# Performance work log

Hardware: AMD Instinct MI355X
Metric: run time of the kernel (lower is better)

## Reference

```python
import jax, jax.numpy as jnp
import numpy as np

CHUNK_SIZE = 256


def setup_inputs() -> dict:
    key = jax.random.key(0)
    kq, kk, kv = jax.random.split(key, 3)
    b, h, L, d, dv = 2, 16, 4096, 16, 64
    return {
        "q": jax.random.normal(kq, (b, h, L, d), dtype=jnp.float32),
        "k": jax.random.normal(kk, (b, h, L, d), dtype=jnp.float32),
        "v": jax.random.normal(kv, (b, h, L, dv), dtype=jnp.float32),
    }


def reference(q, k, v):
    b, h, L, d = q.shape
    dv = v.shape[-1]
    cs = CHUNK_SIZE
    n = L // cs

    q = q * d ** (-0.5)

    # ---- normalizer z over full sequence ----
    k_cumsum = jnp.cumsum(k, axis=-2)                               # [b,h,L,d]
    kk_cumsum = jnp.cumsum(k[..., :, None] * k[..., None, :], axis=-3)  # [b,h,L,d,d]
    z = (q * k_cumsum).sum(-1)
    z = z + 0.5 * jnp.einsum('bhld,bhle,bhlde->bhl', q, q, kk_cumsum)
    z = z + (jnp.arange(L, dtype=z.dtype) + 1.0)[None, None, :]

    # ---- zeroth-order term ----
    o_const = jnp.cumsum(v, axis=-2)                                # [b,h,L,dv]

    # ---- chunked view ----
    qc = q.reshape(b, h, n, cs, d)
    kc = k.reshape(b, h, n, cs, d)
    vc = v.reshape(b, h, n, cs, dv)

    # intra-chunk quadratic attention: S + 0.5*S^2, causal-masked
    s = jnp.einsum('bhnqd,bhnkd->bhnqk', qc, kc)                    # [b,h,n,cs,cs]
    s = s + 0.5 * s ** 2
    causal_mask = jnp.tril(jnp.ones((cs, cs), dtype=bool))
    s = jnp.where(causal_mask, s, jnp.zeros((), dtype=s.dtype))
    o = jnp.einsum('bhnqk,bhnkf->bhnqf', s, vc)                     # [b,h,n,cs,dv]

    # inter-chunk quadratic state: cumulative K x K x V from previous chunks
    kv_quad = jnp.einsum('bhncd,bhnce,bhncf->bhndef', kc, kc, vc)   # [b,h,n,d,d,dv]
    kv_quad = jnp.cumsum(kv_quad, axis=2)
    kv_quad = jnp.concatenate(
        [jnp.zeros_like(kv_quad[:, :, :1]), kv_quad[:, :, :-1]], axis=2)
    o = o + 0.5 * jnp.einsum('bhndef,bhncd,bhnce->bhncf', kv_quad, qc, qc)

    # inter-chunk linear state: cumulative K x V from previous chunks
    kv_lin = jnp.einsum('bhncd,bhnce->bhnde', kc, vc)               # [b,h,n,d,dv]
    kv_lin = jnp.cumsum(kv_lin, axis=2)
    kv_lin = jnp.concatenate(
        [jnp.zeros_like(kv_lin[:, :, :1]), kv_lin[:, :, :-1]], axis=2)
    o = o + jnp.einsum('bhnde,bhncd->bhnce', kv_lin, qc)

    o = o.reshape(b, h, L, dv) + o_const
    return o / (z[..., None] + 1e-6)
```

## Files before the change

kernel.cpp:

```cpp
#include <hip/hip_runtime.h>
#include <hip/hip_cooperative_groups.h>
#include <cstddef>

#define BH    32
#define LSEQ  4096
#define D     16
#define DV    64
#define CS    256
#define NC    16
#define NF    160
#define NZ    65
#define KSTEPS 5
#define PER   (NZ * NF)

typedef short short8 __attribute__((ext_vector_type(8)));
typedef float f32x4 __attribute__((ext_vector_type(4)));

#define OFF_KBF 0u
#define OFF_VT  (4u*1024u*1024u)
#define OFF_ST  (OFF_VT + (unsigned)(BH*NZ*LSEQ*2))

__device__ __forceinline__ unsigned f2bf(float x) {
  unsigned u = __float_as_uint(x);
  return (u + 0x7FFFu + ((u >> 16) & 1u)) >> 16;
}
__device__ __forceinline__ float bf2f(unsigned short u) {
  return __uint_as_float(((unsigned)u) << 16);
}
__device__ __forceinline__ short8 zero8() {
  short8 z = {0,0,0,0,0,0,0,0};
  return z;
}

__device__ __forceinline__ unsigned feat_tbl(int f) {
  if (f == 0)  return 16u | (16u << 8);
  if (f <= 16) return (unsigned)(f - 1) | (16u << 8);
  if (f < 137) {
    int p = f - 17, off = 0;
    for (int d = 0; d < 15; ++d) {
      int cnt = 15 - d;
      if (p < off + cnt) return (unsigned)d | ((unsigned)(d + 1 + p - off) << 8);
      off += cnt;
    }
  }
  if (f < 153) {
    int d = f - 137;
    return (unsigned)d | ((unsigned)d << 8) | (1u << 16);
  }
  return 17u | (17u << 8);
}

struct Smem {
  float kxqx[CS][18];
  __align__(16) unsigned short vt[NZ][264];
  union {
    __align__(16) unsigned short stt[NZ][168];
    struct {
      __align__(16) unsigned short ptile[8][1280];
      float zline[CS];
    } u;
  } b;
  unsigned tbl[NF];
};

__global__ __launch_bounds__(512, 4) void unified(const float* __restrict__ q,
                                                  const float* __restrict__ k,
                                                  const float* __restrict__ v,
                                                  unsigned* __restrict__ kbf_u32,
                                                  unsigned short* __restrict__ st,
                                                  float* __restrict__ out) {
  __shared__ Smem sm;
  int blk = blockIdx.x, bh = blk >> 4, c = blk & 15;
  int t = threadIdx.x, w = t >> 6, lane = t & 63, quad = lane >> 4, n16 = lane & 15;
  const size_t base = (size_t)bh * LSEQ + (size_t)c * CS;

  {
    const float2* kc2 = (const float2*)(k + base * D);
    unsigned* kbd = kbf_u32 + base * D / 2;
    for (int i = t; i < 2048; i += 512) {
      float2 v2 = kc2[i];
      kbd[i] = f2bf(v2.x) | (f2bf(v2.y) << 16);
      int j = i >> 3, dd = (i & 7) * 2;
      sm.kxqx[j][dd] = v2.x; sm.kxqx[j][dd + 1] = v2.y;
    }
    for (int i = t; i < CS; i += 512) { sm.kxqx[i][16] = 1.f; sm.kxqx[i][17] = 0.f; }
    const float* vb = v + base * DV;
    for (int i = t; i < CS * DV; i += 512) {
      int j = i >> 6, f = i & 63;
      sm.vt[f][j] = (unsigned short)f2bf(vb[i]);
    }
    for (int i = t; i < CS; i += 512) sm.vt[64][i] = (unsigned short)0x3F80;
    if (t < NF) sm.tbl[t] = feat_tbl(t);
  }
  __syncthreads();

  if (c < 15 && w < 5) {
    f32x4 acc[2][5];
#pragma unroll
    for (int mm = 0; mm < 2; ++mm)
#pragma unroll
      for (int nt = 0; nt < 5; ++nt) acc[mm][nt] = (f32x4){0.f, 0.f, 0.f, 0.f};
    for (int jt = 0; jt < 8; ++jt) {
      short8 afr[2];
#pragma unroll
      for (int mm = 0; mm < 2; ++mm) {
        int feat = (w * 2 + mm) * 16 + n16;
        unsigned tv = sm.tbl[feat];
        int d = tv & 255, e = (tv >> 8) & 255;
        short8 a;
#pragma unroll
        for (int i = 0; i < 8; ++i) {
          int jj = jt * 32 + quad * 8 + i;
          a[i] = (short)f2bf(sm.kxqx[jj][d] * sm.kxqx[jj][e]);
        }
        afr[mm] = a;
      }
#pragma unroll
      for (int nt = 0; nt < 5; ++nt) {
        int ncol = nt * 16 + n16;
        short8 b = zero8();
        if (ncol < NZ) b = *(const short8*)(&sm.vt[ncol][jt * 32 + quad * 8]);
        acc[0][nt] = __builtin_amdgcn_mfma_f32_16x16x32_bf16(afr[0], b, acc[0][nt], 0, 0, 0);
        acc[1][nt] = __builtin_amdgcn_mfma_f32_16x16x32_bf16(afr[1], b, acc[1][nt], 0, 0, 0);
      }
    }
    unsigned short* stc = st + (size_t)(bh * NC + c) * PER;
#pragma unroll
    for (int mm = 0; mm < 2; ++mm)
#pragma unroll
      for (int nt = 0; nt < 5; ++nt) {
        int col = nt * 16 + n16;
        if (col < NZ) {
          unsigned lo = f2bf(acc[mm][nt][0]) | (f2bf(acc[mm][nt][1]) << 16);
          unsigned hi = f2bf(acc[mm][nt][2]) | (f2bf(acc[mm][nt][3]) << 16);
          int feat0 = (w * 2 + mm) * 16 + quad * 4;
          *(uint2*)(stc + (size_t)col * NF + feat0) = make_uint2(lo, hi);
        }
      }
  }
  __syncthreads();

  {
    const float* qc = q + base * D;
    for (int i = t; i < CS * D; i += 512) {
      int row = i >> 4, dd = i & 15;
      sm.kxqx[row][dd] = qc[i] * 0.25f;
    }
  }

  cooperative_groups::this_grid().sync();

  if (c > 0) {
    const unsigned short* stg = st + (size_t)bh * NC * PER;
    float s0[8], s1[8], s2[8];
#pragma unroll
    for (int e = 0; e < 8; ++e) { s0[e] = 0.f; s1[e] = 0.f; s2[e] = 0.f; }
    const int i0 = t * 8, i1 = i0 + 4096, i2 = i0 + 8192;
    const bool h2 = (i2 < PER);
    for (int cc = 0; cc < c; ++cc) {
      const unsigned short* pcc = stg + (size_t)cc * PER;
      short8 a0 = *(const short8*)(pcc + i0);
      short8 a1 = *(const short8*)(pcc + i1);
      short8 a2 = h2 ? *(const short8*)(pcc + i2) : zero8();
#pragma unroll
      for (int e = 0; e < 8; ++e) {
        s0[e] += bf2f((unsigned short)a0[e]);
        s1[e] += bf2f((unsigned short)a1[e]);
        s2[e] += bf2f((unsigned short)a2[e]);
      }
    }
    {
      int col = i0 / NF, ft = i0 - col * NF;
      short8 p;
#pragma unroll
      for (int e = 0; e < 8; ++e) p[e] = (short)f2bf(s0[e]);
      *(short8*)(&sm.b.stt[col][ft]) = p;
      col = i1 / NF; ft = i1 - col * NF;
#pragma unroll
      for (int e = 0; e < 8; ++e) p[e] = (short)f2bf(s1[e]);
      *(short8*)(&sm.b.stt[col][ft]) = p;
      if (h2) {
        col = i2 / NF; ft = i2 - col * NF;
#pragma unroll
        for (int e = 0; e < 8; ++e) p[e] = (short)f2bf(s2[e]);
        *(short8*)(&sm.b.stt[col][ft]) = p;
      }
    }
  }
  __syncthreads();

  f32x4 acc[2][5];
#pragma unroll
  for (int mm = 0; mm < 2; ++mm)
#pragma unroll
    for (int nt = 0; nt < 5; ++nt) acc[mm][nt] = (f32x4){0.f, 0.f, 0.f, 0.f};

  if (c > 0) {
    for (int ks = 0; ks < KSTEPS; ++ks) {
      short8 afr[2];
#pragma unroll
      for (int mm = 0; mm < 2; ++mm) {
        const float* qrow = sm.kxqx[(w * 2 + mm) * 16 + n16];
        short8 a;
#pragma unroll
        for (int i = 0; i < 8; ++i) {
          int f = ks * 32 + quad * 8 + i;
          unsigned tv = sm.tbl[f];
          float val = qrow[tv & 255] * qrow[(tv >> 8) & 255];
          if (tv & 0x10000u) val *= 0.5f;
          a[i] = (short)f2bf(val);
        }
        afr[mm] = a;
      }
#pragma unroll
      for (int nt = 0; nt < 5; ++nt) {
        int ncol = nt * 16 + n16;
        short8 b = zero8();
        if (ncol < NZ) b = *(const short8*)(&sm.b.stt[ncol][ks * 32 + quad * 8]);
        acc[0][nt] = __builtin_amdgcn_mfma_f32_16x16x32_bf16(afr[0], b, acc[0][nt], 0, 0, 0);
        acc[1][nt] = __builtin_amdgcn_mfma_f32_16x16x32_bf16(afr[1], b, acc[1][nt], 0, 0, 0);
      }
    }
  }
  __syncthreads();

  short8 qfr[2];
#pragma unroll
  for (int mm = 0; mm < 2; ++mm) {
    int m = (w * 2 + mm) * 16 + n16;
    short8 a = zero8();
    if (quad < 2) {
#pragma unroll
      for (int i = 0; i < 8; ++i) a[i] = (short)f2bf(sm.kxqx[m][quad * 8 + i]);
    }
    qfr[mm] = a;
  }
  const unsigned short* kbc = (const unsigned short*)kbf_u32 + base * D;
  unsigned short* pw = &sm.b.u.ptile[w][0];
  short8 ones;
#pragma unroll
  for (int i = 0; i < 8; ++i) ones[i] = (short)0x3F80;

  for (int jt = 0; jt <= w; ++jt) {
    short8 kb[2];
#pragma unroll
    for (int ntk = 0; ntk < 2; ++ntk) {
      short8 b = zero8();
      if (quad < 2)
        b = *(const short8*)(kbc + (size_t)(jt * 32 + ntk * 16 + n16) * D + quad * 8);
      kb[ntk] = b;
    }
    f32x4 zf = (f32x4){0.f, 0.f, 0.f, 0.f};
    f32x4 s[2][2];
#pragma unroll
    for (int mm = 0; mm < 2; ++mm)
#pragma unroll
      for (int ntk = 0; ntk < 2; ++ntk)
        s[mm][ntk] = __builtin_amdgcn_mfma_f32_16x16x32_bf16(qfr[mm], kb[ntk], zf, 0, 0, 0);
    bool diag = (jt == w);
#pragma unroll
    for (int mm = 0; mm < 2; ++mm)
#pragma unroll
      for (int ntk = 0; ntk < 2; ++ntk)
#pragma unroll
        for (int r = 0; r < 4; ++r) {
          float sv = s[mm][ntk][r];
          float phi = fmaf(0.5f * sv, sv, sv) + 1.0f;
          if (diag) {
            int qrow = mm * 16 + quad * 4 + r;
            int kcol = ntk * 16 + n16;
            if (kcol > qrow) phi = 0.f;
          }
          pw[(mm * 16 + quad * 4 + r) * 40 + ntk * 16 + n16] = (unsigned short)f2bf(phi);
        }
    short8 pa[2];
#pragma unroll
    for (int mm = 0; mm < 2; ++mm)
      pa[mm] = *(const short8*)(pw + (mm * 16 + n16) * 40 + quad * 8);
#pragma unroll
    for (int nt = 0; nt < 5; ++nt) {
      int ncol = nt * 16 + n16;
      short8 b;
      if (ncol < 64)       b = *(const short8*)(&sm.vt[ncol][jt * 32 + quad * 8]);
      else if (ncol == 64) b = ones;
      else                 b = zero8();
      acc[0][nt] = __builtin_amdgcn_mfma_f32_16x16x32_bf16(pa[0], b, acc[0][nt], 0, 0, 0);
      acc[1][nt] = __builtin_amdgcn_mfma_f32_16x16x32_bf16(pa[1], b, acc[1][nt], 0, 0, 0);
    }
  }

  if (n16 == 0) {
#pragma unroll
    for (int mm = 0; mm < 2; ++mm)
#pragma unroll
      for (int r = 0; r < 4; ++r)
        sm.b.u.zline[(w * 2 + mm) * 16 + quad * 4 + r] = acc[mm][4][r];
  }
  float* oc = out + base * DV;
#pragma unroll
  for (int mm = 0; mm < 2; ++mm)
#pragma unroll
    for (int r = 0; r < 4; ++r) {
      int qrow = (w * 2 + mm) * 16 + quad * 4 + r;
      float inv = 1.0f / (sm.b.u.zline[qrow] + 1e-6f);
#pragma unroll
      for (int nt = 0; nt < 4; ++nt)
        oc[(size_t)qrow * DV + nt * 16 + n16] = acc[mm][nt][r] * inv;
    }
}

__global__ __launch_bounds__(320) void pass_a(const float* __restrict__ k,
                                              const float* __restrict__ v,
                                              unsigned* __restrict__ kbf_u32,
                                              unsigned* __restrict__ vt_u32,
                                              unsigned short* __restrict__ st) {
  __shared__ float kx[CS][18];
  __shared__ __align__(16) unsigned short vt_lds[NZ][264];
  __shared__ unsigned tbl[NF];
  int blk = blockIdx.x, bh = blk >> 4, c = blk & 15;
  int t = threadIdx.x, w = t >> 6, lane = t & 63, quad = lane >> 4, n16 = lane & 15;
  {
    const float2* kc2 = (const float2*)(k + ((size_t)bh * LSEQ + c * CS) * D);
    unsigned* kbd = kbf_u32 + ((size_t)bh * LSEQ + c * CS) * D / 2;
    for (int i = t; i < 2048; i += 320) {
      float2 v2 = kc2[i];
      kbd[i] = f2bf(v2.x) | (f2bf(v2.y) << 16);
      int j = i >> 3, dd = (i & 7) * 2;
      kx[j][dd] = v2.x; kx[j][dd + 1] = v2.y;
    }
    for (int i = t; i < CS; i += 320) { kx[i][16] = 1.f; kx[i][17] = 0.f; }
  }
  {
    const float* vb = v + ((size_t)bh * LSEQ + c * CS) * DV;
    for (int i = t; i < CS * DV; i += 320) {
      int j = i >> 6, f = i & 63;
      vt_lds[f][j] = (unsigned short)f2bf(vb[i]);
    }
    for (int i = t; i < CS; i += 320) vt_lds[64][i] = (unsigned short)0x3F80;
  }
  if (t < NF) tbl[t] = feat_tbl(t);
  __syncthreads();
  {
    unsigned* vtg = vt_u32 + (size_t)bh * NZ * (LSEQ / 2) + c * (CS / 2);
    for (int i = t; i < NZ * (CS / 2); i += 320) {
      int f = i >> 7, jp = (i & 127) * 2;
      vtg[(size_t)f * (LSEQ / 2) + (i & 127)] =
          (unsigned)vt_lds[f][jp] | ((unsigned)vt_lds[f][jp + 1] << 16);
    }
  }
  f32x4 acc[2][5];
#pragma unroll
  for (int mm = 0; mm < 2; ++mm)
#pragma unroll
    for (int nt = 0; nt < 5; ++nt) acc[mm][nt] = (f32x4){0.f, 0.f, 0.f, 0.f};
  for (int jt = 0; jt < 8; ++jt) {
    short8 afr[2];
#pragma unroll
    for (int mm = 0; mm < 2; ++mm) {
      int feat = (w * 2 + mm) * 16 + n16;
      unsigned tv = tbl[feat];
      int d = tv & 255, e = (tv >> 8) & 255;
      short8 a;
#pragma unroll
      for (int i = 0; i < 8; ++i) {
        int jj = jt * 32 + quad * 8 + i;
        a[i] = (short)f2bf(kx[jj][d] * kx[jj][e]);
      }
      afr[mm] = a;
    }
#pragma unroll
    for (int nt = 0; nt < 5; ++nt) {
      int ncol = nt * 16 + n16;
      short8 b = zero8();
      if (ncol < NZ) b = *(const short8*)(&vt_lds[ncol][jt * 32 + quad * 8]);
      acc[0][nt] = __builtin_amdgcn_mfma_f32_16x16x32_bf16(afr[0], b, acc[0][nt], 0, 0, 0);
      acc[1][nt] = __builtin_amdgcn_mfma_f32_16x16x32_bf16(afr[1], b, acc[1][nt], 0, 0, 0);
    }
  }
  unsigned short* stc = st + (size_t)(bh * NC + c) * PER;
#pragma unroll
  for (int mm = 0; mm < 2; ++mm)
#pragma unroll
    for (int nt = 0; nt < 5; ++nt) {
      int col = nt * 16 + n16;
      if (col < NZ) {
        unsigned lo = f2bf(acc[mm][nt][0]) | (f2bf(acc[mm][nt][1]) << 16);
        unsigned hi = f2bf(acc[mm][nt][2]) | (f2bf(acc[mm][nt][3]) << 16);
        int feat0 = (w * 2 + mm) * 16 + quad * 4;
        *(uint2*)(stc + (size_t)col * NF + feat0) = make_uint2(lo, hi);
      }
    }
}

__global__ __launch_bounds__(256) void pass_b(unsigned short* __restrict__ st) {
  const int TOT = BH * PER;
  int idx = blockIdx.x * 256 + threadIdx.x;
  if (idx >= TOT) return;
  int bh = idx / PER, r = idx - bh * PER;
  unsigned short* p = st + (size_t)bh * NC * PER + r;
  float run = 0.f;
#pragma unroll
  for (int c = 0; c < NC; ++c) {
    unsigned short uv = p[(size_t)c * PER];
    float val = bf2f(uv);
    p[(size_t)c * PER] = (unsigned short)f2bf(run);
    run += val;
  }
}

__global__ __launch_bounds__(512) void pass_c(const float* __restrict__ q,
                                              const unsigned short* __restrict__ kbf,
                                              const unsigned short* __restrict__ vt,
                                              const unsigned short* __restrict__ st,
                                              float* __restrict__ out) {
  __shared__ float qx[CS][18];
  __shared__ unsigned tbl[NF];
  __shared__ __align__(16) unsigned short ptile[8][32 * 40];
  __shared__ float zline[CS];
  int blk = blockIdx.x, bh = blk >> 4, c = blk & 15;
  const size_t base = (size_t)bh * LSEQ + (size_t)c * CS;
  const float* qc = q + base * D;
  int t = threadIdx.x, w = t >> 6, lane = t & 63, quad = lane >> 4, n16 = lane & 15;
  for (int i = t; i < CS * D; i += 512) {
    int row = i >> 4, dd = i & 15;
    qx[row][dd] = qc[i] * 0.25f;
  }
  for (int i = t; i < CS; i += 512) { qx[i][16] = 1.f; qx[i][17] = 0.f; }
  if (t < NF) tbl[t] = feat_tbl(t);
  __syncthreads();
  f32x4 acc[2][5];
#pragma unroll
  for (int mm = 0; mm < 2; ++mm)
#pragma unroll
    for (int nt = 0; nt < 5; ++nt) acc[mm][nt] = (f32x4){0.f, 0.f, 0.f, 0.f};
  if (c > 0) {
    const unsigned short* stc = st + (size_t)(bh * NC + c) * PER;
    for (int ks = 0; ks < KSTEPS; ++ks) {
      short8 afr[2];
#pragma unroll
      for (int mm = 0; mm < 2; ++mm) {
        const float* qrow = qx[(w * 2 + mm) * 16 + n16];
        short8 a;
#pragma unroll
        for (int i = 0; i < 8; ++i) {
          int f = ks * 32 + quad * 8 + i;
          unsigned tv = tbl[f];
          float val = qrow[tv & 255] * qrow[(tv >> 8) & 255];
          if (tv & 0x10000u) val *= 0.5f;
          a[i] = (short)f2bf(val);
        }
        afr[mm] = a;
      }
#pragma unroll
      for (int nt = 0; nt < 5; ++nt) {
        int ncol = nt * 16 + n16;
        short8 b = zero8();
        if (ncol < NZ) b = *(const short8*)(stc + (size_t)ncol * NF + ks * 32 + quad * 8);
        acc[0][nt] = __builtin_amdgcn_mfma_f32_16x16x32_bf16(afr[0], b, acc[0][nt], 0, 0, 0);
        acc[1][nt] = __builtin_amdgcn_mfma_f32_16x16x32_bf16(afr[1], b, acc[1][nt], 0, 0, 0);
      }
    }
  }
  short8 qfr[2];
#pragma unroll
  for (int mm = 0; mm < 2; ++mm) {
    int m = (w * 2 + mm) * 16 + n16;
    short8 a = zero8();
    if (quad < 2) {
#pragma unroll
      for (int i = 0; i < 8; ++i) a[i] = (short)f2bf(qx[m][quad * 8 + i]);
    }
    qfr[mm] = a;
  }
  const unsigned short* kbc = kbf + base * D;
  const unsigned short* vtb = vt + (size_t)bh * NZ * LSEQ + (size_t)c * CS;
  unsigned short* pw = &ptile[w][0];
  short8 ones;
#pragma unroll
  for (int i = 0; i < 8; ++i) ones[i] = (short)0x3F80;
  for (int jt = 0; jt <= w; ++jt) {
    short8 kb[2];
#pragma unroll
    for (int ntk = 0; ntk < 2; ++ntk) {
      short8 b = zero8();
      if (quad < 2)
        b = *(const short8*)(kbc + (size_t)(jt * 32 + ntk * 16 + n16) * D + quad * 8);
      kb[ntk] = b;
    }
    f32x4 zf = (f32x4){0.f, 0.f, 0.f, 0.f};
    f32x4 s[2][2];
#pragma unroll
    for (int mm = 0; mm < 2; ++mm)
#pragma unroll
      for (int ntk = 0; ntk < 2; ++ntk)
        s[mm][ntk] = __builtin_amdgcn_mfma_f32_16x16x32_bf16(qfr[mm], kb[ntk], zf, 0, 0, 0);
    bool diag = (jt == w);
#pragma unroll
    for (int mm = 0; mm < 2; ++mm)
#pragma unroll
      for (int ntk = 0; ntk < 2; ++ntk)
#pragma unroll
        for (int r = 0; r < 4; ++r) {
          float sv = s[mm][ntk][r];
          float phi = fmaf(0.5f * sv, sv, sv) + 1.0f;
          if (diag) {
            int qrow = mm * 16 + quad * 4 + r;
            int kcol = ntk * 16 + n16;
            if (kcol > qrow) phi = 0.f;
          }
          pw[(mm * 16 + quad * 4 + r) * 40 + ntk * 16 + n16] = (unsigned short)f2bf(phi);
        }
    short8 pa[2];
#pragma unroll
    for (int mm = 0; mm < 2; ++mm)
      pa[mm] = *(const short8*)(pw + (mm * 16 + n16) * 40 + quad * 8);
#pragma unroll
    for (int nt = 0; nt < 5; ++nt) {
      int ncol = nt * 16 + n16;
      short8 b;
      if (ncol < 64)       b = *(const short8*)(vtb + (size_t)ncol * LSEQ + jt * 32 + quad * 8);
      else if (ncol == 64) b = ones;
      else                 b = zero8();
      acc[0][nt] = __builtin_amdgcn_mfma_f32_16x16x32_bf16(pa[0], b, acc[0][nt], 0, 0, 0);
      acc[1][nt] = __builtin_amdgcn_mfma_f32_16x16x32_bf16(pa[1], b, acc[1][nt], 0, 0, 0);
    }
  }
  if (n16 == 0) {
#pragma unroll
    for (int mm = 0; mm < 2; ++mm)
#pragma unroll
      for (int r = 0; r < 4; ++r)
        zline[(w * 2 + mm) * 16 + quad * 4 + r] = acc[mm][4][r];
  }
  float* oc = out + base * DV;
#pragma unroll
  for (int mm = 0; mm < 2; ++mm)
#pragma unroll
    for (int r = 0; r < 4; ++r) {
      int qrow = (w * 2 + mm) * 16 + quad * 4 + r;
      float inv = 1.0f / (zline[qrow] + 1e-6f);
#pragma unroll
      for (int nt = 0; nt < 4; ++nt)
        oc[(size_t)qrow * DV + nt * 16 + n16] = acc[mm][nt][r] * inv;
    }
}

extern "C" void kernel_launch(void* const* d_in, const int* in_sizes, int n_in,
                              void* d_out, int out_size, void* d_ws, size_t ws_size,
                              hipStream_t stream) {
  (void)in_sizes; (void)n_in; (void)out_size; (void)ws_size;
  const float* q = (const float*)d_in[0];
  const float* k = (const float*)d_in[1];
  const float* v = (const float*)d_in[2];
  float* out = (float*)d_out;
  char* wsb = (char*)d_ws;
  unsigned*       kbf32 = (unsigned*)(wsb + OFF_KBF);
  unsigned short* kbf   = (unsigned short*)(wsb + OFF_KBF);
  unsigned*       vt32  = (unsigned*)(wsb + OFF_VT);
  unsigned short* vtp   = (unsigned short*)(wsb + OFF_VT);
  unsigned short* stp   = (unsigned short*)(wsb + OFF_ST);

  int nb = 0;
  hipError_t oe = hipOccupancyMaxActiveBlocksPerMultiprocessor(
      &nb, reinterpret_cast<const void*>(unified), 512, 0);
  if (oe == hipSuccess && nb >= 2) {
    void* args[] = {(void*)&q, (void*)&k, (void*)&v,
                    (void*)&kbf32, (void*)&stp, (void*)&out};
    hipLaunchCooperativeKernel(reinterpret_cast<const void*>(unified),
                               dim3(BH * NC), dim3(512), args, 0, stream);
  } else {
    pass_a<<<BH * NC, 320, 0, stream>>>(k, v, kbf32, vt32, stp);
    pass_b<<<1300, 256, 0, stream>>>(stp);
    pass_c<<<BH * NC, 512, 0, stream>>>(q, kbf, vtp, stp, out);
  }
}
```

Baseline: 130.2 us.

## Use packed bf16 conversion, vectorized loads, MFMA priority hints and fast reciprocal

Replaces the software float-to-bf16 rounding with the v_cvt_pk_bf16_f32 instruction throughout. Staging of K, V and Q into shared memory now uses float4 vector loads, with K/Q rows padded to 20 floats and V transposed two rows at a time into packed pairs. Feature-table lookups are hoisted out of the inner loops, and the 0.5 factor for diagonal features moves from the query-side feature build to the chunk-state store. MFMA blocks are wrapped in s_setprio, and the final normalization uses a hardware reciprocal. Together these aim to cut VALU and LDS instruction overhead around the matrix ops, at the cost of slightly looser precision in the reciprocal.

Result: slower. 135.2 us (+3.9%).

```diff
diff --git a/kernel.cpp b/kernel.cpp
--- a/kernel.cpp
+++ b/kernel.cpp
@@ -12,9 +12,12 @@
 #define NZ    65
 #define KSTEPS 5
 #define PER   (NZ * NF)
+#define QXS   20
 
 typedef short short8 __attribute__((ext_vector_type(8)));
 typedef float f32x4 __attribute__((ext_vector_type(4)));
+typedef float f4 __attribute__((ext_vector_type(4)));
+typedef unsigned uint4v __attribute__((ext_vector_type(4)));
 
 #define OFF_KBF 0u
 #define OFF_VT  (4u*1024u*1024u)
@@ -30,6 +33,15 @@
 __device__ __forceinline__ short8 zero8() {
   short8 z = {0,0,0,0,0,0,0,0};
   return z;
+}
+__device__ __forceinline__ unsigned cvtpk(float lo, float hi) {
+  unsigned r;
+  asm("v_cvt_pk_bf16_f32 %0, %1, %2" : "=v"(r) : "v"(lo), "v"(hi));
+  return r;
+}
+__device__ __forceinline__ short8 pk4(unsigned a, unsigned b, unsigned c, unsigned d) {
+  uint4v u = {a, b, c, d};
+  return __builtin_bit_cast(short8, u);
 }
 
 __device__ __forceinline__ unsigned feat_tbl(int f) {
@@ -51,7 +63,7 @@
 }
 
 struct Smem {
-  float kxqx[CS][18];
+  float kxqx[CS][QXS];
   __align__(16) unsigned short vt[NZ][264];
   union {
     __align__(16) unsigned short stt[NZ][168];
@@ -75,76 +87,88 @@
   const size_t base = (size_t)bh * LSEQ + (size_t)c * CS;
 
   {
-    const float2* kc2 = (const float2*)(k + base * D);
-    unsigned* kbd = kbf_u32 + base * D / 2;
-    for (int i = t; i < 2048; i += 512) {
-      float2 v2 = kc2[i];
-      kbd[i] = f2bf(v2.x) | (f2bf(v2.y) << 16);
-      int j = i >> 3, dd = (i & 7) * 2;
-      sm.kxqx[j][dd] = v2.x; sm.kxqx[j][dd + 1] = v2.y;
-    }
-    for (int i = t; i < CS; i += 512) { sm.kxqx[i][16] = 1.f; sm.kxqx[i][17] = 0.f; }
-    const float* vb = v + base * DV;
-    for (int i = t; i < CS * DV; i += 512) {
-      int j = i >> 6, f = i & 63;
-      sm.vt[f][j] = (unsigned short)f2bf(vb[i]);
-    }
-    for (int i = t; i < CS; i += 512) sm.vt[64][i] = (unsigned short)0x3F80;
+    const f4* K4 = (const f4*)(k + base * D);
+    uint2* kbd2 = (uint2*)(kbf_u32 + base * D / 2);
+    for (int idx = t; idx < 1024; idx += 512) {
+      f4 kv = K4[idx];
+      kbd2[idx] = make_uint2(cvtpk(kv[0], kv[1]), cvtpk(kv[2], kv[3]));
+      *(f4*)&sm.kxqx[idx >> 2][(idx & 3) * 4] = kv;
+    }
+    for (int i = t; i < CS; i += 512)
+      *(float2*)&sm.kxqx[i][16] = make_float2(1.f, 0.f);
+    const f4* V4 = (const f4*)(v + base * DV);
+    for (int idx = t; idx < 2048; idx += 512) {
+      int m16 = idx & 15, j0 = (idx >> 4) * 2;
+      f4 a  = V4[j0 * 16 + m16];
+      f4 bq = V4[j0 * 16 + 16 + m16];
+#pragma unroll
+      for (int r = 0; r < 4; ++r)
+        *(unsigned*)&sm.vt[m16 * 4 + r][j0] = cvtpk(a[r], bq[r]);
+    }
+    if (t < 128) ((unsigned*)&sm.vt[64][0])[t] = 0x3F803F80u;
     if (t < NF) sm.tbl[t] = feat_tbl(t);
   }
   __syncthreads();
 
   if (c < 15 && w < 5) {
+    unsigned tv0 = sm.tbl[(w * 2 + 0) * 16 + n16];
+    unsigned tv1 = sm.tbl[(w * 2 + 1) * 16 + n16];
+    int d0 = tv0 & 255, e0 = (tv0 >> 8) & 255;
+    int d1 = tv1 & 255, e1 = (tv1 >> 8) & 255;
     f32x4 acc[2][5];
 #pragma unroll
     for (int mm = 0; mm < 2; ++mm)
 #pragma unroll
       for (int nt = 0; nt < 5; ++nt) acc[mm][nt] = (f32x4){0.f, 0.f, 0.f, 0.f};
     for (int jt = 0; jt < 8; ++jt) {
-      short8 afr[2];
-#pragma unroll
-      for (int mm = 0; mm < 2; ++mm) {
-        int feat = (w * 2 + mm) * 16 + n16;
-        unsigned tv = sm.tbl[feat];
-        int d = tv & 255, e = (tv >> 8) & 255;
-        short8 a;
-#pragma unroll
-        for (int i = 0; i < 8; ++i) {
-          int jj = jt * 32 + quad * 8 + i;
-          a[i] = (short)f2bf(sm.kxqx[jj][d] * sm.kxqx[jj][e]);
-        }
-        afr[mm] = a;
-      }
+      float x0[8], x1[8];
+#pragma unroll
+      for (int i = 0; i < 8; ++i) {
+        const float* kr = &sm.kxqx[jt * 32 + quad * 8 + i][0];
+        x0[i] = kr[d0] * kr[e0];
+        x1[i] = kr[d1] * kr[e1];
+      }
+      short8 afr0 = pk4(cvtpk(x0[0], x0[1]), cvtpk(x0[2], x0[3]),
+                        cvtpk(x0[4], x0[5]), cvtpk(x0[6], x0[7]));
+      short8 afr1 = pk4(cvtpk(x1[0], x1[1]), cvtpk(x1[2], x1[3]),
+                        cvtpk(x1[4], x1[5]), cvtpk(x1[6], x1[7]));
+      __builtin_amdgcn_s_setprio(1);
 #pragma unroll
       for (int nt = 0; nt < 5; ++nt) {
         int ncol = nt * 16 + n16;
         short8 b = zero8();
         if (ncol < NZ) b = *(const short8*)(&sm.vt[ncol][jt * 32 + quad * 8]);
-        acc[0][nt] = __builtin_amdgcn_mfma_f32_16x16x32_bf16(afr[0], b, acc[0][nt], 0, 0, 0);
-        acc[1][nt] = __builtin_amdgcn_mfma_f32_16x16x32_bf16(afr[1], b, acc[1][nt], 0, 0, 0);
-      }
+        acc[0][nt] = __builtin_amdgcn_mfma_f32_16x16x32_bf16(afr0, b, acc[0][nt], 0, 0, 0);
+        acc[1][nt] = __builtin_amdgcn_mfma_f32_16x16x32_bf16(afr1, b, acc[1][nt], 0, 0, 0);
+      }
+      __builtin_amdgcn_s_setprio(0);
     }
     unsigned short* stc = st + (size_t)(bh * NC + c) * PER;
 #pragma unroll
-    for (int mm = 0; mm < 2; ++mm)
+    for (int mm = 0; mm < 2; ++mm) {
+      int feat0 = (w * 2 + mm) * 16 + quad * 4;
+      float sc[4];
+#pragma unroll
+      for (int r = 0; r < 4; ++r)
+        sc[r] = (feat0 + r >= 137 && feat0 + r < 153) ? 0.5f : 1.0f;
 #pragma unroll
       for (int nt = 0; nt < 5; ++nt) {
         int col = nt * 16 + n16;
         if (col < NZ) {
-          unsigned lo = f2bf(acc[mm][nt][0]) | (f2bf(acc[mm][nt][1]) << 16);
-          unsigned hi = f2bf(acc[mm][nt][2]) | (f2bf(acc[mm][nt][3]) << 16);
-          int feat0 = (w * 2 + mm) * 16 + quad * 4;
+          unsigned lo = cvtpk(acc[mm][nt][0] * sc[0], acc[mm][nt][1] * sc[1]);
+          unsigned hi = cvtpk(acc[mm][nt][2] * sc[2], acc[mm][nt][3] * sc[3]);
           *(uint2*)(stc + (size_t)col * NF + feat0) = make_uint2(lo, hi);
         }
       }
+    }
   }
   __syncthreads();
 
   {
-    const float* qc = q + base * D;
-    for (int i = t; i < CS * D; i += 512) {
-      int row = i >> 4, dd = i & 15;
-      sm.kxqx[row][dd] = qc[i] * 0.25f;
+    const f4* Q4 = (const f4*)(q + base * D);
+    for (int idx = t; idx < 1024; idx += 512) {
+      f4 qv = Q4[idx] * 0.25f;
+      *(f4*)&sm.kxqx[idx >> 2][(idx & 3) * 4] = qv;
     }
   }
 
@@ -171,19 +195,18 @@
     }
     {
       int col = i0 / NF, ft = i0 - col * NF;
-      short8 p;
-#pragma unroll
-      for (int e = 0; e < 8; ++e) p[e] = (short)f2bf(s0[e]);
-      *(short8*)(&sm.b.stt[col][ft]) = p;
+      *(short8*)(&sm.b.stt[col][ft]) =
+          pk4(cvtpk(s0[0], s0[1]), cvtpk(s0[2], s0[3]),
+              cvtpk(s0[4], s0[5]), cvtpk(s0[6], s0[7]));
       col = i1 / NF; ft = i1 - col * NF;
-#pragma unroll
-      for (int e = 0; e < 8; ++e) p[e] = (short)f2bf(s1[e]);
-      *(short8*)(&sm.b.stt[col][ft]) = p;
+      *(short8*)(&sm.b.stt[col][ft]) =
+          pk4(cvtpk(s1[0], s1[1]), cvtpk(s1[2], s1[3]),
+              cvtpk(s1[4], s1[5]), cvtpk(s1[6], s1[7]));
       if (h2) {
         col = i2 / NF; ft = i2 - col * NF;
-#pragma unroll
-        for (int e = 0; e < 8; ++e) p[e] = (short)f2bf(s2[e]);
-        *(short8*)(&sm.b.stt[col][ft]) = p;
+        *(short8*)(&sm.b.stt[col][ft]) =
+            pk4(cvtpk(s2[0], s2[1]), cvtpk(s2[2], s2[3]),
+                cvtpk(s2[4], s2[5]), cvtpk(s2[6], s2[7]));
       }
     }
   }
@@ -196,30 +219,33 @@
     for (int nt = 0; nt < 5; ++nt) acc[mm][nt] = (f32x4){0.f, 0.f, 0.f, 0.f};
 
   if (c > 0) {
+    const float* qrow0 = &sm.kxqx[(w * 2 + 0) * 16 + n16][0];
+    const float* qrow1 = &sm.kxqx[(w * 2 + 1) * 16 + n16][0];
     for (int ks = 0; ks < KSTEPS; ++ks) {
-      short8 afr[2];
-#pragma unroll
-      for (int mm = 0; mm < 2; ++mm) {
-        const float* qrow = sm.kxqx[(w * 2 + mm) * 16 + n16];
-        short8 a;
-#pragma unroll
-        for (int i = 0; i < 8; ++i) {
-          int f = ks * 32 + quad * 8 + i;
-          unsigned tv = sm.tbl[f];
-          float val = qrow[tv & 255] * qrow[(tv >> 8) & 255];
-          if (tv & 0x10000u) val *= 0.5f;
-          a[i] = (short)f2bf(val);
-        }
-        afr[mm] = a;
-      }
+      unsigned tvv[8];
+#pragma unroll
+      for (int i = 0; i < 8; ++i) tvv[i] = sm.tbl[ks * 32 + quad * 8 + i];
+      float x0[8], x1[8];
+#pragma unroll
+      for (int i = 0; i < 8; ++i) {
+        int d = tvv[i] & 255, e = (tvv[i] >> 8) & 255;
+        x0[i] = qrow0[d] * qrow0[e];
+        x1[i] = qrow1[d] * qrow1[e];
+      }
+      short8 afr0 = pk4(cvtpk(x0[0], x0[1]), cvtpk(x0[2], x0[3]),
+                        cvtpk(x0[4], x0[5]), cvtpk(x0[6], x0[7]));
+      short8 afr1 = pk4(cvtpk(x1[0], x1[1]), cvtpk(x1[2], x1[3]),
+                        cvtpk(x1[4], x1[5]), cvtpk(x1[6], x1[7]));
+      __builtin_amdgcn_s_setprio(1);
 #pragma unroll
       for (int nt = 0; nt < 5; ++nt) {
         int ncol = nt * 16 + n16;
         short8 b = zero8();
         if (ncol < NZ) b = *(const short8*)(&sm.b.stt[ncol][ks * 32 + quad * 8]);
-        acc[0][nt] = __builtin_amdgcn_mfma_f32_16x16x32_bf16(afr[0], b, acc[0][nt], 0, 0, 0);
-        acc[1][nt] = __builtin_amdgcn_mfma_f32_16x16x32_bf16(afr[1], b, acc[1][nt], 0, 0, 0);
-      }
+        acc[0][nt] = __builtin_amdgcn_mfma_f32_16x16x32_bf16(afr0, b, acc[0][nt], 0, 0, 0);
+        acc[1][nt] = __builtin_amdgcn_mfma_f32_16x16x32_bf16(afr1, b, acc[1][nt], 0, 0, 0);
+      }
+      __builtin_amdgcn_s_setprio(0);
     }
   }
   __syncthreads();
@@ -230,8 +256,11 @@
     int m = (w * 2 + mm) * 16 + n16;
     short8 a = zero8();
     if (quad < 2) {
-#pragma unroll
-      for (int i = 0; i < 8; ++i) a[i] = (short)f2bf(sm.kxqx[m][quad * 8 + i]);
+      const float* qr = &sm.kxqx[m][quad * 8];
+      f4 q0 = *(const f4*)(qr);
+      f4 q1 = *(const f4*)(qr + 4);
+      a = pk4(cvtpk(q0[0], q0[1]), cvtpk(q0[2], q0[3]),
+              cvtpk(q1[0], q1[1]), cvtpk(q1[2], q1[3]));
     }
     qfr[mm] = a;
   }
@@ -252,31 +281,43 @@
     }
     f32x4 zf = (f32x4){0.f, 0.f, 0.f, 0.f};
     f32x4 s[2][2];
+    __builtin_amdgcn_s_setprio(1);
 #pragma unroll
     for (int mm = 0; mm < 2; ++mm)
 #pragma unroll
       for (int ntk = 0; ntk < 2; ++ntk)
         s[mm][ntk] = __builtin_amdgcn_mfma_f32_16x16x32_bf16(qfr[mm], kb[ntk], zf, 0, 0, 0);
+    __builtin_amdgcn_s_setprio(0);
     bool diag = (jt == w);
 #pragma unroll
     for (int mm = 0; mm < 2; ++mm)
 #pragma unroll
-      for (int ntk = 0; ntk < 2; ++ntk)
+      for (int ntk = 0; ntk < 2; ++ntk) {
+        float ph[4];
 #pragma unroll
         for (int r = 0; r < 4; ++r) {
           float sv = s[mm][ntk][r];
-          float phi = fmaf(0.5f * sv, sv, sv) + 1.0f;
+          float phi = fmaf(sv, fmaf(0.5f, sv, 1.0f), 1.0f);
           if (diag) {
             int qrow = mm * 16 + quad * 4 + r;
             int kcol = ntk * 16 + n16;
             if (kcol > qrow) phi = 0.f;
           }
-          pw[(mm * 16 + quad * 4 + r) * 40 + ntk * 16 + n16] = (unsigned short)f2bf(phi);
+          ph[r] = phi;
         }
+        unsigned u01 = cvtpk(ph[0], ph[1]);
+        unsigned u23 = cvtpk(ph[2], ph[3]);
+        int rb = (mm * 16 + quad * 4) * 40 + ntk * 16 + n16;
+        pw[rb      ] = (unsigned short)u01;
+        pw[rb +  40] = (unsigned short)(u01 >> 16);
+        pw[rb +  80] = (unsigned short)u23;
+        pw[rb + 120] = (unsigned short)(u23 >> 16);
+      }
     short8 pa[2];
 #pragma unroll
     for (int mm = 0; mm < 2; ++mm)
       pa[mm] = *(const short8*)(pw + (mm * 16 + n16) * 40 + quad * 8);
+    __builtin_amdgcn_s_setprio(1);
 #pragma unroll
     for (int nt = 0; nt < 5; ++nt) {
       int ncol = nt * 16 + n16;
@@ -287,6 +328,7 @@
       acc[0][nt] = __builtin_amdgcn_mfma_f32_16x16x32_bf16(pa[0], b, acc[0][nt], 0, 0, 0);
       acc[1][nt] = __builtin_amdgcn_mfma_f32_16x16x32_bf16(pa[1], b, acc[1][nt], 0, 0, 0);
     }
+    __builtin_amdgcn_s_setprio(0);
   }
 
   if (n16 == 0) {
@@ -302,7 +344,7 @@
 #pragma unroll
     for (int r = 0; r < 4; ++r) {
       int qrow = (w * 2 + mm) * 16 + quad * 4 + r;
-      float inv = 1.0f / (sm.b.u.zline[qrow] + 1e-6f);
+      float inv = __builtin_amdgcn_rcpf(sm.b.u.zline[qrow] + 1e-6f);
 #pragma unroll
       for (int nt = 0; nt < 4; ++nt)
         oc[(size_t)qrow * DV + nt * 16 + n16] = acc[mm][nt][r] * inv;
```
